# Kernel tuning notes

Measured on AMD Instinct MI355X. Metric: run time of the kernel, lower is better.

Reference implementation:

```python
import jax, jax.numpy as jnp
import numpy as np

N = 2097152
N_LAYERS = 32
N_SUB = 8


def setup_inputs() -> dict:
    key = jax.random.key(0)
    k1, k2, k3, k4 = jax.random.split(key, 4)
    return {
        "x": jax.random.normal(k1, (N, 2), dtype=jnp.float32),
        "act_w": 0.05 * jax.random.normal(k2, (N_LAYERS,), dtype=jnp.float32),
        "bias_b": 0.05 * jax.random.normal(k3, (N_LAYERS, 2), dtype=jnp.float32),
        "lin_w": 0.05 * jax.random.normal(k4, (N_LAYERS, N_SUB), dtype=jnp.float32),
    }


def _forward_chain(q, p, act_w, bias_b, lin_w):
    # Apply Modules[0..end] with inverse=0.
    n_layers, n_sub = lin_w.shape
    for i in range(n_layers):
        # activation module: up adds w*tanh(p) to q, low adds w*tanh(q) to p
        if i % 2 == 0:
            q = q + act_w[i] * jnp.tanh(p)
        else:
            p = p + act_w[i] * jnp.tanh(q)
        # bias module (inserted at j == 0)
        q = q + bias_b[i, 0]
        p = p + bias_b[i, 1]
        # linear shear modules
        for j in range(n_sub):
            if j % 2 == 0:   # linear_module_up: q += w*p
                q = q + lin_w[i, j] * p
            else:            # linear_module_low: p += w*q
                p = p + lin_w[i, j] * q
    return q, p


def _inverse_chain(q, p, act_w, bias_b, lin_w):
    # Apply all modules in reverse order with inverse=1 (negated weights).
    n_layers, n_sub = lin_w.shape
    for i in reversed(range(n_layers)):
        for j in reversed(range(n_sub)):
            if j % 2 == 0:
                q = q - lin_w[i, j] * p
            else:
                p = p - lin_w[i, j] * q
        q = q - bias_b[i, 0]
        p = p - bias_b[i, 1]
        if i % 2 == 0:
            q = q - act_w[i] * jnp.tanh(p)
        else:
            p = p - act_w[i] * jnp.tanh(q)
    return q, p


def reference(x, act_w, bias_b, lin_w):
    q, p = x[..., 0], x[..., 1]
    q, p = _forward_chain(q, p, act_w, bias_b, lin_w)
    # time reversal: multiply by [1, -1]
    p = -p
    q, p = _inverse_chain(q, p, act_w, bias_b, lin_w)
    # final module-0 inverse is included in _inverse_chain; scale by [1, -1]
    return jnp.stack([q, -p], axis=-1)
```

## Files before the change

kernel.cpp:

```cpp
#include <hip/hip_runtime.h>

constexpr int NL = 32;
constexpr int PPT = 4;

__device__ __forceinline__ float fast_tanh(float x) {
    float e = __expf(2.0f * x);
    float r = __builtin_amdgcn_rcpf(e + 1.0f);
    return fmaf(-2.0f, r, 1.0f);
}

__global__ __launch_bounds__(256) void sympnet_kernel(
    const float* __restrict__ x,
    const float* __restrict__ act_w,
    const float* __restrict__ bias_b,
    const float* __restrict__ lin_w,
    float* __restrict__ out,
    int nthreads_total)
{
    __shared__ float sf[NL][8];
    __shared__ float si[NL][8];

    int t = threadIdx.x;
    if (t < NL) {
        float m00 = 1.f, m01 = 0.f, m10 = 0.f, m11 = 1.f;
        #pragma unroll
        for (int j = 0; j < 8; ++j) {
            float w = lin_w[t * 8 + j];
            if ((j & 1) == 0) {
                m00 = fmaf(w, m10, m00); m01 = fmaf(w, m11, m01);
            } else {
                m10 = fmaf(w, m00, m10); m11 = fmaf(w, m01, m11);
            }
        }
        float b0 = bias_b[2 * t], b1 = bias_b[2 * t + 1];
        float aw = act_w[t];
        sf[t][0] = m00; sf[t][1] = m01; sf[t][2] = m10; sf[t][3] = m11;
        sf[t][4] = fmaf(m00, b0, m01 * b1);
        sf[t][5] = fmaf(m10, b0, m11 * b1);
        sf[t][6] = aw; sf[t][7] = 0.f;
        si[t][0] = m11; si[t][1] = -m01; si[t][2] = -m10; si[t][3] = m00;
        si[t][4] = -b0; si[t][5] = -b1; si[t][6] = aw; si[t][7] = 0.f;
    }
    __syncthreads();

    int gid = blockIdx.x * blockDim.x + t;
    if (gid >= nthreads_total) return;

    const float4* x4 = (const float4*)x;
    float4 v0 = x4[2 * gid];
    float4 v1 = x4[2 * gid + 1];
    float q[PPT] = {v0.x, v0.z, v1.x, v1.z};
    float p[PPT] = {v0.y, v0.w, v1.y, v1.w};

    #pragma unroll 1
    for (int i = 0; i < NL; i += 2) {
        float4 M = *(const float4*)&sf[i][0];
        float4 C = *(const float4*)&sf[i][4];
        #pragma unroll
        for (int k = 0; k < PPT; ++k) {
            float qq = fmaf(C.z, fast_tanh(p[k]), q[k]);
            float nq = fmaf(M.y, p[k], C.x); nq = fmaf(M.x, qq, nq);
            float np = fmaf(M.w, p[k], C.y); np = fmaf(M.z, qq, np);
            q[k] = nq; p[k] = np;
        }
        float4 M2 = *(const float4*)&sf[i + 1][0];
        float4 C2 = *(const float4*)&sf[i + 1][4];
        #pragma unroll
        for (int k = 0; k < PPT; ++k) {
            float pp = fmaf(C2.z, fast_tanh(q[k]), p[k]);
            float nq = fmaf(M2.y, pp, C2.x); nq = fmaf(M2.x, q[k], nq);
            float np = fmaf(M2.w, pp, C2.y); np = fmaf(M2.z, q[k], np);
            q[k] = nq; p[k] = np;
        }
    }

    #pragma unroll
    for (int k = 0; k < PPT; ++k) p[k] = -p[k];

    #pragma unroll 1
    for (int i = NL - 1; i >= 0; i -= 2) {
        float4 M = *(const float4*)&si[i][0];
        float4 C = *(const float4*)&si[i][4];
        #pragma unroll
        for (int k = 0; k < PPT; ++k) {
            float nq = fmaf(M.x, q[k], C.x); nq = fmaf(M.y, p[k], nq);
            float np = fmaf(M.z, q[k], C.y); np = fmaf(M.w, p[k], np);
            np = fmaf(-C.z, fast_tanh(nq), np);
            q[k] = nq; p[k] = np;
        }
        float4 M2 = *(const float4*)&si[i - 1][0];
        float4 C2 = *(const float4*)&si[i - 1][4];
        #pragma unroll
        for (int k = 0; k < PPT; ++k) {
            float nq = fmaf(M2.x, q[k], C2.x); nq = fmaf(M2.y, p[k], nq);
            float np = fmaf(M2.z, q[k], C2.y); np = fmaf(M2.w, p[k], np);
            nq = fmaf(-C2.z, fast_tanh(np), nq);
            q[k] = nq; p[k] = np;
        }
    }

    float4 o0 = {q[0], -p[0], q[1], -p[1]};
    float4 o1 = {q[2], -p[2], q[3], -p[3]};
    float4* out4 = (float4*)out;
    out4[2 * gid] = o0;
    out4[2 * gid + 1] = o1;
}

extern "C" void kernel_launch(void* const* d_in, const int* in_sizes, int n_in,
                              void* d_out, int out_size, void* d_ws, size_t ws_size,
                              hipStream_t stream) {
    const float* x      = (const float*)d_in[0];
    const float* act_w  = (const float*)d_in[1];
    const float* bias_b = (const float*)d_in[2];
    const float* lin_w  = (const float*)d_in[3];
    float* out = (float*)d_out;

    int npts = in_sizes[0] / 2;
    int nthreads = npts / PPT;
    int blocks = (nthreads + 255) / 256;
    sympnet_kernel<<<blocks, 256, 0, stream>>>(x, act_w, bias_b, lin_w, out, nthreads);
}
```

Baseline: 108.3 us.

## Rescale state to fold tanh into exp2/rcp and precompute layer tables

Scales q,p by 2/ln2 so each tanh becomes exp2 plus rcp, with the tanh constant folded into per-layer bias constants. A separate tiny kernel builds the per-layer tables in workspace, so the main kernel reads them from global/scalar memory instead of rebuilding them in LDS with a sync. Points per thread go from 4 to 8 and each loop body fuses both layer halves. The cost is an extra kernel launch, more register pressure, fewer threads, and removal of the bounds check.

```diff
diff --git a/kernel.cpp b/kernel.cpp
--- a/kernel.cpp
+++ b/kernel.cpp
@@ -1,109 +1,120 @@
 #include <hip/hip_runtime.h>
 
 constexpr int NL = 32;
-constexpr int PPT = 4;
+constexpr int PPT = 8;
 
-__device__ __forceinline__ float fast_tanh(float x) {
-    float e = __expf(2.0f * x);
-    float r = __builtin_amdgcn_rcpf(e + 1.0f);
-    return fmaf(-2.0f, r, 1.0f);
+#define C_SCALE 2.8853900817779268f
+#define INV_C   0.34657359027997264f
+
+__device__ __forceinline__ float fast_exp2(float x) {
+#if __has_builtin(__builtin_amdgcn_exp2f)
+    return __builtin_amdgcn_exp2f(x);
+#else
+    return __expf(0.69314718055994531f * x);
+#endif
 }
 
-__global__ __launch_bounds__(256) void sympnet_kernel(
+__global__ void build_tables(const float* __restrict__ act_w,
+                             const float* __restrict__ bias_b,
+                             const float* __restrict__ lin_w,
+                             float* __restrict__ tab)
+{
+    int t = threadIdx.x;
+    if (t >= NL) return;
+    float m00 = 1.f, m01 = 0.f, m10 = 0.f, m11 = 1.f;
+    #pragma unroll
+    for (int j = 0; j < 8; ++j) {
+        float w = lin_w[t * 8 + j];
+        if ((j & 1) == 0) { m00 = fmaf(w, m10, m00); m01 = fmaf(w, m11, m01); }
+        else              { m10 = fmaf(w, m00, m10); m11 = fmaf(w, m01, m11); }
+    }
+    float b0 = bias_b[2 * t], b1 = bias_b[2 * t + 1];
+    float aw = act_w[t];
+    const float c = C_SCALE;
+    float awc = aw * c;
+
+    float C0 = c * fmaf(m00, b0, m01 * b1);
+    float C1 = c * fmaf(m10, b0, m11 * b1);
+    if ((t & 1) == 0) { C0 = fmaf(awc, m00, C0); C1 = fmaf(awc, m10, C1); }
+    else              { C0 = fmaf(awc, m01, C0); C1 = fmaf(awc, m11, C1); }
+    float* f = &tab[t * 16];
+    f[0] = m00; f[1] = m01; f[2] = m10; f[3] = m11;
+    f[4] = C0;  f[5] = C1;  f[6] = -2.f * awc; f[7] = 0.f;
+
+    float i00 = m11, i01 = -m01, i10 = -m10, i11 = m00;
+    float D0 = -c * b0, D1 = -c * b1;
+    if ((t & 1) == 0) D0 -= awc; else D1 -= awc;
+    f[8]  = i00; f[9]  = i01; f[10] = i10; f[11] = i11;
+    f[12] = D0;  f[13] = D1;  f[14] = 2.f * awc; f[15] = 0.f;
+}
+
+__global__ __launch_bounds__(256) void sympnet_main(
     const float* __restrict__ x,
-    const float* __restrict__ act_w,
-    const float* __restrict__ bias_b,
-    const float* __restrict__ lin_w,
-    float* __restrict__ out,
-    int nthreads_total)
+    const float* __restrict__ tab,
+    float* __restrict__ out)
 {
-    __shared__ float sf[NL][8];
-    __shared__ float si[NL][8];
+    int gid = blockIdx.x * blockDim.x + threadIdx.x;
+    const float4* x4 = (const float4*)x;
+    float4* out4 = (float4*)out;
+    long base = (long)gid * (PPT / 2);
 
-    int t = threadIdx.x;
-    if (t < NL) {
-        float m00 = 1.f, m01 = 0.f, m10 = 0.f, m11 = 1.f;
-        #pragma unroll
-        for (int j = 0; j < 8; ++j) {
-            float w = lin_w[t * 8 + j];
-            if ((j & 1) == 0) {
-                m00 = fmaf(w, m10, m00); m01 = fmaf(w, m11, m01);
-            } else {
-                m10 = fmaf(w, m00, m10); m11 = fmaf(w, m01, m11);
-            }
-        }
-        float b0 = bias_b[2 * t], b1 = bias_b[2 * t + 1];
-        float aw = act_w[t];
-        sf[t][0] = m00; sf[t][1] = m01; sf[t][2] = m10; sf[t][3] = m11;
-        sf[t][4] = fmaf(m00, b0, m01 * b1);
-        sf[t][5] = fmaf(m10, b0, m11 * b1);
-        sf[t][6] = aw; sf[t][7] = 0.f;
-        si[t][0] = m11; si[t][1] = -m01; si[t][2] = -m10; si[t][3] = m00;
-        si[t][4] = -b0; si[t][5] = -b1; si[t][6] = aw; si[t][7] = 0.f;
+    float Q[PPT], P[PPT];
+    #pragma unroll
+    for (int k = 0; k < PPT / 2; ++k) {
+        float4 v = x4[base + k];
+        Q[2*k]   = C_SCALE * v.x; P[2*k]   = C_SCALE * v.y;
+        Q[2*k+1] = C_SCALE * v.z; P[2*k+1] = C_SCALE * v.w;
     }
-    __syncthreads();
-
-    int gid = blockIdx.x * blockDim.x + t;
-    if (gid >= nthreads_total) return;
-
-    const float4* x4 = (const float4*)x;
-    float4 v0 = x4[2 * gid];
-    float4 v1 = x4[2 * gid + 1];
-    float q[PPT] = {v0.x, v0.z, v1.x, v1.z};
-    float p[PPT] = {v0.y, v0.w, v1.y, v1.w};
 
     #pragma unroll 1
     for (int i = 0; i < NL; i += 2) {
-        float4 M = *(const float4*)&sf[i][0];
-        float4 C = *(const float4*)&sf[i][4];
+        const float* f = &tab[i * 16];
+        float m00=f[0], m01=f[1], m10=f[2], m11=f[3], C0=f[4], C1=f[5], T=f[6];
+        const float* g = &tab[(i + 1) * 16];
+        float n00=g[0], n01=g[1], n10=g[2], n11=g[3], E0=g[4], E1=g[5], U=g[6];
         #pragma unroll
         for (int k = 0; k < PPT; ++k) {
-            float qq = fmaf(C.z, fast_tanh(p[k]), q[k]);
-            float nq = fmaf(M.y, p[k], C.x); nq = fmaf(M.x, qq, nq);
-            float np = fmaf(M.w, p[k], C.y); np = fmaf(M.z, qq, np);
-            q[k] = nq; p[k] = np;
-        }
-        float4 M2 = *(const float4*)&sf[i + 1][0];
-        float4 C2 = *(const float4*)&sf[i + 1][4];
-        #pragma unroll
-        for (int k = 0; k < PPT; ++k) {
-            float pp = fmaf(C2.z, fast_tanh(q[k]), p[k]);
-            float nq = fmaf(M2.y, pp, C2.x); nq = fmaf(M2.x, q[k], nq);
-            float np = fmaf(M2.w, pp, C2.y); np = fmaf(M2.z, q[k], np);
-            q[k] = nq; p[k] = np;
+            float r  = __builtin_amdgcn_rcpf(fast_exp2(P[k]) + 1.0f);
+            float Qa = fmaf(T, r, Q[k]);
+            float Qn = fmaf(m00, Qa, fmaf(m01, P[k], C0));
+            float Pn = fmaf(m10, Qa, fmaf(m11, P[k], C1));
+            float r2 = __builtin_amdgcn_rcpf(fast_exp2(Qn) + 1.0f);
+            float Pa = fmaf(U, r2, Pn);
+            Q[k] = fmaf(n00, Qn, fmaf(n01, Pa, E0));
+            P[k] = fmaf(n10, Qn, fmaf(n11, Pa, E1));
         }
     }
 
     #pragma unroll
-    for (int k = 0; k < PPT; ++k) p[k] = -p[k];
+    for (int k = 0; k < PPT; ++k) P[k] = -P[k];
 
     #pragma unroll 1
-    for (int i = NL - 1; i >= 0; i -= 2) {
-        float4 M = *(const float4*)&si[i][0];
-        float4 C = *(const float4*)&si[i][4];
+    for (int i = NL - 1; i > 0; i -= 2) {
+        const float* g = &tab[i * 16 + 8];
+        float n00=g[0], n01=g[1], n10=g[2], n11=g[3], E0=g[4], E1=g[5], U=g[6];
+        const float* f = &tab[(i - 1) * 16 + 8];
+        float m00=f[0], m01=f[1], m10=f[2], m11=f[3], C0=f[4], C1=f[5], T=f[6];
         #pragma unroll
         for (int k = 0; k < PPT; ++k) {
-            float nq = fmaf(M.x, q[k], C.x); nq = fmaf(M.y, p[k], nq);
-            float np = fmaf(M.z, q[k], C.y); np = fmaf(M.w, p[k], np);
-            np = fmaf(-C.z, fast_tanh(nq), np);
-            q[k] = nq; p[k] = np;
-        }
-        float4 M2 = *(const float4*)&si[i - 1][0];
-        float4 C2 = *(const float4*)&si[i - 1][4];
-        #pragma unroll
-        for (int k = 0; k < PPT; ++k) {
-            float nq = fmaf(M2.x, q[k], C2.x); nq = fmaf(M2.y, p[k], nq);
-            float np = fmaf(M2.z, q[k], C2.y); np = fmaf(M2.w, p[k], np);
-            nq = fmaf(-C2.z, fast_tanh(np), nq);
-            q[k] = nq; p[k] = np;
+            float Qn = fmaf(n00, Q[k], fmaf(n01, P[k], E0));
+            float Pn = fmaf(n10, Q[k], fmaf(n11, P[k], E1));
+            float r  = __builtin_amdgcn_rcpf(fast_exp2(Qn) + 1.0f);
+            Pn = fmaf(U, r, Pn);
+            float Q2 = fmaf(m00, Qn, fmaf(m01, Pn, C0));
+            float P2 = fmaf(m10, Qn, fmaf(m11, Pn, C1));
+            float r2 = __builtin_amdgcn_rcpf(fast_exp2(P2) + 1.0f);
+            Q[k] = fmaf(T, r2, Q2);
+            P[k] = P2;
         }
     }
 
-    float4 o0 = {q[0], -p[0], q[1], -p[1]};
-    float4 o1 = {q[2], -p[2], q[3], -p[3]};
-    float4* out4 = (float4*)out;
-    out4[2 * gid] = o0;
-    out4[2 * gid + 1] = o1;
+    #pragma unroll
+    for (int k = 0; k < PPT / 2; ++k) {
+        float4 o;
+        o.x =  INV_C * Q[2*k];   o.y = -INV_C * P[2*k];
+        o.z =  INV_C * Q[2*k+1]; o.w = -INV_C * P[2*k+1];
+        out4[base + k] = o;
+    }
 }
 
 extern "C" void kernel_launch(void* const* d_in, const int* in_sizes, int n_in,
@@ -114,9 +125,12 @@
     const float* bias_b = (const float*)d_in[2];
     const float* lin_w  = (const float*)d_in[3];
     float* out = (float*)d_out;
+    float* tab = (float*)d_ws;
+
+    build_tables<<<1, 64, 0, stream>>>(act_w, bias_b, lin_w, tab);
 
     int npts = in_sizes[0] / 2;
     int nthreads = npts / PPT;
     int blocks = (nthreads + 255) / 256;
-    sympnet_kernel<<<blocks, 256, 0, stream>>>(x, act_w, bias_b, lin_w, out, nthreads);
+    sympnet_main<<<blocks, 256, 0, stream>>>(x, tab, out);
 }
```

New measurement: 104.0 us. 1.04x faster.
